# Kernel tuning notes

Hardware: AMD Instinct MI355X
Metric: run time of the kernel (lower is better)

The kernel has to match this reference:

```python
import jax, jax.numpy as jnp
import numpy as np

N, E, C_IN, C_OUT, K = 50000, 800000, 64, 64, 3

def setup_inputs() -> dict:
    key = jax.random.key(0)
    k1, k2, k3, k4, k5, k6 = jax.random.split(key, 6)
    x = jax.random.normal(k1, (N, C_IN), dtype=jnp.float32)
    row = jax.random.randint(k2, (E,), 0, N)
    col = jax.random.randint(k3, (E,), 0, N)
    # PyG ChebConv removes self loops; avoid generating them
    col = jnp.where(col == row, (col + 1) % N, col)
    edge_index = jnp.stack([row, col])
    edge_weight = jax.random.uniform(k4, (E,), dtype=jnp.float32)
    # ChebConv learned params: one [C_in, C_out] matrix per Chebyshev order, plus bias
    W = jax.random.normal(k5, (K, C_IN, C_OUT), dtype=jnp.float32) / np.sqrt(C_IN).astype(np.float32)
    b = jax.random.normal(k6, (C_OUT,), dtype=jnp.float32) * 0.01
    return {"x": x, "edge_index": edge_index, "edge_weight": edge_weight, "W": W, "b": b}


def reference(x, edge_index, edge_weight, W, b):
    row, col = edge_index[0], edge_index[1]
    # PyG ChebConv.__norm__ with sym normalization and lambda_max = 2.0:
    # L_hat = (2/lambda_max) * (I - D^{-1/2} A D^{-1/2}) - I = -D^{-1/2} A D^{-1/2}
    deg = jax.ops.segment_sum(edge_weight, row, num_segments=N)
    dis = jnp.where(deg > 0, jax.lax.rsqrt(deg), 0.0)  # deg_inv_sqrt, inf -> 0
    w = -dis[row] * edge_weight * dis[col]             # [E] normalized Laplacian weights

    def prop(h):  # sparse matvec: L_hat @ h, [N, C]
        return jax.ops.segment_sum(w[:, None] * h[col], row, num_segments=N)

    # Chebyshev recurrence: T0 = x, T1 = L_hat x, Tk = 2 L_hat T_{k-1} - T_{k-2}
    Tx0 = x
    out = Tx0 @ W[0]
    Tx1 = prop(Tx0)
    out = out + Tx1 @ W[1]
    for k in range(2, K):
        Tx2 = 2.0 * prop(Tx1) - Tx0
        out = out + Tx2 @ W[k]
        Tx0, Tx1 = Tx1, Tx2
    return jax.nn.relu(out + b)
```

## Files before the change

### kernel.cpp

```cpp
#include <hip/hip_runtime.h>
#include <hip/hip_bf16.h>

#define C 64
#define EPB 4096
#define BKTCAP 8192
#define BKTSH 13

typedef unsigned short u16;
typedef unsigned int u32;
typedef unsigned long long u64;

__device__ __forceinline__ u16 f2bf_rne(float v) {
    unsigned u = __float_as_uint(v);
    u += 0x7FFFu + ((u >> 16) & 1u);
    return (u16)(u >> 16);
}
__device__ __forceinline__ float bf2f(u16 u) {
    return __uint_as_float((unsigned)u << 16);
}


__global__ __launch_bounds__(256) void buildA_kernel(const int* __restrict__ row,
                                                     const int* __restrict__ col,
                                                     const float* __restrict__ ew,
                                                     u32* __restrict__ Tg,
                                                     u64* __restrict__ pay,
                                                     const float* __restrict__ x,
                                                     u16* __restrict__ xh,
                                                     int E, int total4, int nthreads) {
    __shared__ u32 h[256];
    __shared__ u32 cur[256];
    int t = threadIdx.x;
    int b = blockIdx.x;
    h[t] = 0;
    __syncthreads();
    int base = b * EPB;

    int rcache[EPB / 256];
#pragma unroll
    for (int u = 0; u < EPB / 256; u++) {
        int e = base + u * 256 + t;
        rcache[u] = (e < E) ? row[e] : -1;
        if (rcache[u] >= 0) atomicAdd(&h[rcache[u] >> 8], 1u);
    }
    __syncthreads();
    cur[t] = ((u32)t << BKTSH) + atomicAdd(&Tg[t], h[t]);
    __syncthreads();
#pragma unroll
    for (int u = 0; u < EPB / 256; u++) {
        int e = base + u * 256 + t;
        int r = rcache[u];
        if (r >= 0) {
            u32 c = (u32)col[e];
            u32 rc = ((u32)r << 16) | c;
            u32 pos = atomicAdd(&cur[r >> 8], 1u);
            pay[pos] = ((u64)rc << 32) | (u64)__float_as_uint(ew[e]);
        }
    }

    int gtid = b * 256 + t;
    for (int i = gtid; i < total4; i += nthreads) {
        float4 v = *(const float4*)(x + (size_t)i * 4);
        ushort4 o;
        o.x = f2bf_rne(v.x); o.y = f2bf_rne(v.y);
        o.z = f2bf_rne(v.z); o.w = f2bf_rne(v.w);
        *(ushort4*)(xh + (size_t)i * 4) = o;
    }
}

__global__ __launch_bounds__(256) void p2_kernel(const u64* __restrict__ pay,
                                                 const u32* __restrict__ Tg,
                                                 int* __restrict__ rowptr,
                                                 float* __restrict__ dis,
                                                 float2* __restrict__ ewc,
                                                 int N, int E) {
    __shared__ u32 h[256];
    __shared__ u32 s[256];
    __shared__ u32 cur[256];
    __shared__ float dsum[256];
    __shared__ u32 gbase_s;
    int t = threadIdx.x;
    int bk = blockIdx.x;

    u32 tv = Tg[t];
    s[t] = tv;
    __syncthreads();
    for (int off = 1; off < 256; off <<= 1) {
        u32 u = (t >= off) ? s[t - off] : 0;
        __syncthreads();
        s[t] += u;
        __syncthreads();
    }
    if (t == bk) gbase_s = s[t] - tv;
    if (bk == 0 && t == 0) rowptr[N] = E;
    __syncthreads();
    u32 gbase = gbase_s;
    u32 cnt = Tg[bk];
    u32 pbase = (u32)bk << BKTSH;

    h[t] = 0;
    dsum[t] = 0.0f;
    __syncthreads();
    for (u32 j = t; j < cnt; j += 256) {
        u64 v = pay[pbase + j];
        u32 lr = (u32)(v >> 48) & 255u;
        atomicAdd(&h[lr], 1u);
    }
    __syncthreads();
    u32 hv = h[t];
    s[t] = hv;
    __syncthreads();
    for (int off = 1; off < 256; off <<= 1) {
        u32 u = (t >= off) ? s[t - off] : 0;
        __syncthreads();
        s[t] += u;
        __syncthreads();
    }
    u32 p = s[t] - hv;
    int r = bk * 256 + t;
    if (r < N) rowptr[r] = (int)(gbase + p);
    cur[t] = gbase + p;
    __syncthreads();
    for (u32 j = t; j < cnt; j += 256) {
        u64 v = pay[pbase + j];
        u32 rc = (u32)(v >> 32);
        u32 lr = (rc >> 16) & 255u;
        float w = __uint_as_float((u32)v);
        u32 pos = atomicAdd(&cur[lr], 1u);
        ewc[pos] = make_float2(w, __uint_as_float(rc & 0xffffu));
        atomicAdd(&dsum[lr], w);
    }
    __syncthreads();
    if (r < N) {
        float dv = dsum[t];
        dis[r] = (dv > 0.0f) ? rsqrtf(dv) : 0.0f;
    }
}

template <int NORM>
__global__ __launch_bounds__(256) void spmm_kernel(
        const int* __restrict__ rowptr,
        float2* __restrict__ ewc,
        const float* __restrict__ dis,
        const u64* __restrict__ h64,
        float* __restrict__ out32,
        u64* __restrict__ outbf,
        int N) {
    __shared__ float2 eds[8][32];

    int tid  = threadIdx.x;
    int hw   = tid >> 5;
    int l32  = tid & 31;
    int e2   = l32 >> 4;
    int cq   = l32 & 15;

    int row = blockIdx.x * 8 + hw;
    if (row >= N) return;

    int beg = rowptr[row];
    int end = rowptr[row + 1];
    float disr = NORM ? dis[row] : 0.0f;

    float a0 = 0.f, a1 = 0.f, a2 = 0.f, a3 = 0.f;

    for (int base = beg; base < end; base += 32) {
        int idx = base + l32;
        bool valid = idx < end;
        float2 ed = valid ? ewc[idx] : make_float2(0.0f, __uint_as_float(0));
        if (NORM) {
            u32 c = __float_as_uint(ed.y);
            ed.x = -disr * ed.x * dis[c];
            if (valid) ewc[idx] = ed;
        }
        eds[hw][l32] = ed;
        int cnt = end - base; if (cnt > 32) cnt = 32;
        for (int j = 0; j < cnt; j += 4) {
            float2 f0 = eds[hw][j + e2];
            float2 f1 = eds[hw][j + 2 + e2];
            u64 hv0 = h64[(size_t)__float_as_uint(f0.y) * 16 + cq];
            u64 hv1 = h64[(size_t)__float_as_uint(f1.y) * 16 + cq];
            float w0 = f0.x, w1 = f1.x;
            u32 lo, hi;
            lo = (u32)hv0; hi = (u32)(hv0 >> 32);
            a0 = fmaf(w0, bf2f((u16)(lo & 0xffffu)), a0);
            a1 = fmaf(w0, bf2f((u16)(lo >> 16)),     a1);
            a2 = fmaf(w0, bf2f((u16)(hi & 0xffffu)), a2);
            a3 = fmaf(w0, bf2f((u16)(hi >> 16)),     a3);
            lo = (u32)hv1; hi = (u32)(hv1 >> 32);
            a0 = fmaf(w1, bf2f((u16)(lo & 0xffffu)), a0);
            a1 = fmaf(w1, bf2f((u16)(lo >> 16)),     a1);
            a2 = fmaf(w1, bf2f((u16)(hi & 0xffffu)), a2);
            a3 = fmaf(w1, bf2f((u16)(hi >> 16)),     a3);
        }
    }

    a0 += __shfl_xor(a0, 16);
    a1 += __shfl_xor(a1, 16);
    a2 += __shfl_xor(a2, 16);
    a3 += __shfl_xor(a3, 16);

    if (e2 == 0) {
        *(float4*)(out32 + (size_t)row * C + 4 * cq) = make_float4(a0, a1, a2, a3);
        if (NORM) {
            u32 p0 = (u32)f2bf_rne(a0) | ((u32)f2bf_rne(a1) << 16);
            u32 p1 = (u32)f2bf_rne(a2) | ((u32)f2bf_rne(a3) << 16);
            outbf[(size_t)row * 16 + cq] = (u64)p0 | ((u64)p1 << 32);
        }
    }
}

__global__ __launch_bounds__(256) void final_gemm_kernel(
        const float* __restrict__ x,
        const float* __restrict__ T1,
        const float* __restrict__ P,
        const float* __restrict__ W,
        const float* __restrict__ b,
        float* __restrict__ out, int N) {
    __shared__ float As[16][64];
    __shared__ float Ws[16][64];

    int t  = threadIdx.x;
    int tx = t & 15;
    int ty = t >> 4;
    int n0 = blockIdx.x * 64;

    int sn = t >> 2;
    int skb = (t & 3) * 4;

    float acc[4][4];
#pragma unroll
    for (int i = 0; i < 4; i++)
#pragma unroll
        for (int j = 0; j < 4; j++) acc[i][j] = 0.0f;

#pragma unroll 1
    for (int s = 0; s < 12; s++) {
        float4 wv = *(const float4*)(W + s * 1024 + t * 4);
        int nn = n0 + sn;
        float4 av = make_float4(0.f, 0.f, 0.f, 0.f);
        if (nn < N) {
            if (s < 4) {
                av = *(const float4*)(x + (size_t)nn * C + s * 16 + skb);
            } else if (s < 8) {
                av = *(const float4*)(T1 + (size_t)nn * C + (s - 4) * 16 + skb);
            } else {
                float4 pv = *(const float4*)(P + (size_t)nn * C + (s - 8) * 16 + skb);
                float4 xv = *(const float4*)(x + (size_t)nn * C + (s - 8) * 16 + skb);
                av = make_float4(2.0f * pv.x - xv.x, 2.0f * pv.y - xv.y,
                                 2.0f * pv.z - xv.z, 2.0f * pv.w - xv.w);
            }
        }
        __syncthreads();
        {
            int wk = (t * 4) >> 6;
            int wc = (t * 4) & 63;
            *(float4*)&Ws[wk][wc] = wv;
        }
        As[skb + 0][sn] = av.x;
        As[skb + 1][sn] = av.y;
        As[skb + 2][sn] = av.z;
        As[skb + 3][sn] = av.w;
        __syncthreads();

#pragma unroll
        for (int kk = 0; kk < 16; kk++) {
            float4 a4 = *(const float4*)&As[kk][ty * 4];
            float4 w4 = *(const float4*)&Ws[kk][tx * 4];
            float ar[4] = {a4.x, a4.y, a4.z, a4.w};
            float wr[4] = {w4.x, w4.y, w4.z, w4.w};
#pragma unroll
            for (int i = 0; i < 4; i++)
#pragma unroll
                for (int j = 0; j < 4; j++)
                    acc[i][j] = fmaf(ar[i], wr[j], acc[i][j]);
        }
    }

    float4 bv = *(const float4*)(b + tx * 4);
    float br[4] = {bv.x, bv.y, bv.z, bv.w};
#pragma unroll
    for (int i = 0; i < 4; i++) {
        int node = n0 + ty * 4 + i;
        if (node < N) {
            float4 o;
            o.x = fmaxf(acc[i][0] + br[0], 0.0f);
            o.y = fmaxf(acc[i][1] + br[1], 0.0f);
            o.z = fmaxf(acc[i][2] + br[2], 0.0f);
            o.w = fmaxf(acc[i][3] + br[3], 0.0f);
            *(float4*)(out + (size_t)node * C + tx * 4) = o;
        }
    }
}

extern "C" void kernel_launch(void* const* d_in, const int* in_sizes, int n_in,
                              void* d_out, int out_size, void* d_ws, size_t ws_size,
                              hipStream_t stream) {
    const float* x  = (const float*)d_in[0];
    const int*   ei = (const int*)d_in[1];
    const float* ew = (const float*)d_in[2];
    const float* W  = (const float*)d_in[3];
    const float* b  = (const float*)d_in[4];
    float* out = (float*)d_out;

    const int N = in_sizes[0] / C;
    const int E = in_sizes[2];
    const int* row = ei;
    const int* col = ei + E;

    char* ws = (char*)d_ws;
    size_t off = 0;
    auto alloc = [&](size_t bytes) {
        void* p = ws + off;
        off = (off + bytes + 255) & ~(size_t)255;
        return p;
    };
    const int NB = (E + EPB - 1) / EPB;
    const int NBUCK = (N + 255) / 256;

    float*  dis    = (float*)alloc((size_t)N * 4);
    int*    rowptr = (int*)alloc((size_t)(N + 1) * 4);
    float2* ewc    = (float2*)alloc((size_t)E * 8);
    u64*    pay    = (u64*)alloc((size_t)256 * BKTCAP * 8);
    float*  T1     = (float*)alloc((size_t)N * C * 4);
    float*  P      = (float*)alloc((size_t)N * C * 4);
    u32*    Tg     = (u32*)alloc((size_t)256 * 4);
    u16*    xh     = (u16*)alloc((size_t)N * C * 2);
    u16*    T1h    = (u16*)alloc((size_t)N * C * 2);

    const int B = 256;
    int total4 = N * C / 4;

    hipMemsetAsync(Tg, 0, 256 * 4, stream);

    buildA_kernel<<<NB, B, 0, stream>>>(row, col, ew, Tg, pay, x, xh,
                                        E, total4, NB * B);
    p2_kernel<<<NBUCK, B, 0, stream>>>(pay, Tg, rowptr, dis, ewc, N, E);

    int spmm_blocks = (N + 7) / 8;
    spmm_kernel<1><<<spmm_blocks, B, 0, stream>>>(rowptr, ewc, dis, (const u64*)xh,
                                                  T1, (u64*)T1h, N);
    spmm_kernel<0><<<spmm_blocks, B, 0, stream>>>(rowptr, ewc, dis, (const u64*)T1h,
                                                  P, (u64*)nullptr, N);

    final_gemm_kernel<<<(N + 63) / 64, B, 0, stream>>>(x, T1, P, W, b, out, N);
}
```

Before: 173.4 us.

## Batch neighbor gathers in SpMM and fold Chebyshev combine into weights

The sparse propagation inner loop now reads all 32 staged edge records, then issues up to 16 independent neighbor-row gathers before any of the FMAs. This raises memory-level parallelism and hides gather latency, at the cost of more registers. The final GEMM applies the identity x@W0 + (2P - x)@W2 = x@(W0 - W2) + P@(2W2) by adjusting the weights instead of the activations. That removes the extra x load and elementwise work per node in the last stage, while adding a second small weight load in the first stage.

```diff
diff --git a/kernel.cpp b/kernel.cpp
--- a/kernel.cpp
+++ b/kernel.cpp
@@ -174,23 +174,40 @@
         }
         eds[hw][l32] = ed;
         int cnt = end - base; if (cnt > 32) cnt = 32;
-        for (int j = 0; j < cnt; j += 4) {
-            float2 f0 = eds[hw][j + e2];
-            float2 f1 = eds[hw][j + 2 + e2];
-            u64 hv0 = h64[(size_t)__float_as_uint(f0.y) * 16 + cq];
-            u64 hv1 = h64[(size_t)__float_as_uint(f1.y) * 16 + cq];
-            float w0 = f0.x, w1 = f1.x;
-            u32 lo, hi;
-            lo = (u32)hv0; hi = (u32)(hv0 >> 32);
-            a0 = fmaf(w0, bf2f((u16)(lo & 0xffffu)), a0);
-            a1 = fmaf(w0, bf2f((u16)(lo >> 16)),     a1);
-            a2 = fmaf(w0, bf2f((u16)(hi & 0xffffu)), a2);
-            a3 = fmaf(w0, bf2f((u16)(hi >> 16)),     a3);
-            lo = (u32)hv1; hi = (u32)(hv1 >> 32);
-            a0 = fmaf(w1, bf2f((u16)(lo & 0xffffu)), a0);
-            a1 = fmaf(w1, bf2f((u16)(lo >> 16)),     a1);
-            a2 = fmaf(w1, bf2f((u16)(hi & 0xffffu)), a2);
-            a3 = fmaf(w1, bf2f((u16)(hi >> 16)),     a3);
+
+        float2 fa[8], fb[8];
+#pragma unroll
+        for (int k = 0; k < 8; k++) {
+            if (4 * k < cnt) {
+                fa[k] = eds[hw][4 * k + e2];
+                fb[k] = eds[hw][4 * k + 2 + e2];
+            } else {
+                fa[k] = make_float2(0.0f, __uint_as_float(0));
+                fb[k] = make_float2(0.0f, __uint_as_float(0));
+            }
+        }
+        u64 ha[8], hb[8];
+#pragma unroll
+        for (int k = 0; k < 8; k++) {
+            if (4 * k < cnt) {
+                ha[k] = h64[(size_t)__float_as_uint(fa[k].y) * 16 + cq];
+                hb[k] = h64[(size_t)__float_as_uint(fb[k].y) * 16 + cq];
+            } else {
+                ha[k] = 0; hb[k] = 0;
+            }
+        }
+#pragma unroll
+        for (int k = 0; k < 8; k++) {
+            u32 lo = (u32)ha[k], hi = (u32)(ha[k] >> 32);
+            a0 = fmaf(fa[k].x, bf2f((u16)(lo & 0xffffu)), a0);
+            a1 = fmaf(fa[k].x, bf2f((u16)(lo >> 16)),     a1);
+            a2 = fmaf(fa[k].x, bf2f((u16)(hi & 0xffffu)), a2);
+            a3 = fmaf(fa[k].x, bf2f((u16)(hi >> 16)),     a3);
+            lo = (u32)hb[k]; hi = (u32)(hb[k] >> 32);
+            a0 = fmaf(fb[k].x, bf2f((u16)(lo & 0xffffu)), a0);
+            a1 = fmaf(fb[k].x, bf2f((u16)(lo >> 16)),     a1);
+            a2 = fmaf(fb[k].x, bf2f((u16)(hi & 0xffffu)), a2);
+            a3 = fmaf(fb[k].x, bf2f((u16)(hi >> 16)),     a3);
         }
     }
 
@@ -235,20 +252,22 @@
 
 #pragma unroll 1
     for (int s = 0; s < 12; s++) {
-        float4 wv = *(const float4*)(W + s * 1024 + t * 4);
+        float4 wv;
+        if (s < 4) {
+            float4 w0 = *(const float4*)(W + s * 1024 + t * 4);
+            float4 w2 = *(const float4*)(W + (s + 8) * 1024 + t * 4);
+            wv = make_float4(w0.x - w2.x, w0.y - w2.y, w0.z - w2.z, w0.w - w2.w);
+        } else if (s < 8) {
+            wv = *(const float4*)(W + s * 1024 + t * 4);
+        } else {
+            float4 w2 = *(const float4*)(W + s * 1024 + t * 4);
+            wv = make_float4(2.0f * w2.x, 2.0f * w2.y, 2.0f * w2.z, 2.0f * w2.w);
+        }
         int nn = n0 + sn;
         float4 av = make_float4(0.f, 0.f, 0.f, 0.f);
         if (nn < N) {
-            if (s < 4) {
-                av = *(const float4*)(x + (size_t)nn * C + s * 16 + skb);
-            } else if (s < 8) {
-                av = *(const float4*)(T1 + (size_t)nn * C + (s - 4) * 16 + skb);
-            } else {
-                float4 pv = *(const float4*)(P + (size_t)nn * C + (s - 8) * 16 + skb);
-                float4 xv = *(const float4*)(x + (size_t)nn * C + (s - 8) * 16 + skb);
-                av = make_float4(2.0f * pv.x - xv.x, 2.0f * pv.y - xv.y,
-                                 2.0f * pv.z - xv.z, 2.0f * pv.w - xv.w);
-            }
+            const float* src = (s < 4) ? x : ((s < 8) ? T1 : P);
+            av = *(const float4*)(src + (size_t)nn * C + (s & 3) * 16 + skb);
         }
         __syncthreads();
         {
```

After: 178.9 us. 3.2% more time.
